# Kernel tuning notes

Hardware: AMD Instinct MI355X
Metric: run time of the kernel (lower is better)

The kernel has to match this reference:

```python
import jax, jax.numpy as jnp
import numpy as np

B, T, D = 16, 32, 4096
H, HD = 32, 128          # n_heads, head_dim
MAX_SEQ = 2048
START_POS = 1024


def _rope(x):
    # x: [b, t, h, hd]; faithful to source: positions start at 0 (no start_pos offset)
    t, hd = x.shape[1], x.shape[-1]
    theta = 10000.0 ** (-2.0 * jnp.arange(0, hd, 2, dtype=jnp.float32) / hd)  # [hd/2]
    freqs = jnp.arange(t, dtype=jnp.float32)[:, None] * theta                 # [t, hd/2]
    cos = jnp.repeat(jnp.cos(freqs), 2, axis=-1)[None, :, None, :]            # [1,t,1,hd]
    sin = jnp.repeat(jnp.sin(freqs), 2, axis=-1)[None, :, None, :]
    # rotate: even slots <- -odd, odd slots <- even (interleaved)
    x_rot = jnp.stack([-x[..., 1::2], x[..., 0::2]], axis=-1).reshape(x.shape)
    return x * cos + x_rot * sin


def setup_inputs() -> dict:
    key = jax.random.key(0)
    ks = jax.random.split(key, 7)
    s = 0.02
    return {
        "x": jax.random.normal(ks[0], (B, T, D), dtype=jnp.float32),
        "wq": jax.random.normal(ks[1], (D, D), dtype=jnp.float32) * s,
        "wk": jax.random.normal(ks[2], (D, D), dtype=jnp.float32) * s,
        "wv": jax.random.normal(ks[3], (D, D), dtype=jnp.float32) * s,
        "wo": jax.random.normal(ks[4], (D, D), dtype=jnp.float32) * s,
        "k_cache": jax.random.normal(ks[5], (B, MAX_SEQ, H, HD), dtype=jnp.float32),
        "v_cache": jax.random.normal(ks[6], (B, MAX_SEQ, H, HD), dtype=jnp.float32),
        "start_pos": START_POS,
    }


def reference(x, wq, wk, wv, wo, k_cache, v_cache, start_pos):
    b, t, _ = x.shape
    xq = (x @ wq).reshape(b, t, H, HD)
    xk = (x @ wk).reshape(b, t, H, HD)
    xv = (x @ wv).reshape(b, t, H, HD)
    xq = _rope(xq)
    xk = _rope(xk)
    # KV-cache append (start_pos is a static Python int)
    k_cache = jax.lax.dynamic_update_slice(k_cache, xk, (0, start_pos, 0, 0))
    v_cache = jax.lax.dynamic_update_slice(v_cache, xv, (0, start_pos, 0, 0))
    L = start_pos + t
    keys = k_cache[:, :L]    # [b, L, h, hd]
    values = v_cache[:, :L]
    # n_rep == 1 -> repeat_kv is identity
    scores = jnp.einsum("bthd,bshd->bhts", xq, keys) / np.float32(np.sqrt(HD))
    probs = jax.nn.softmax(scores.astype(jnp.float32), axis=-1).astype(xq.dtype)
    out = jnp.einsum("bhts,bshd->bthd", probs, values).reshape(b, t, H * HD)
    return out @ wo
```

## Files before the change

### kernel.cpp

```cpp
#include <hip/hip_runtime.h>
#include <hip/hip_bf16.h>

#define B_ 16
#define T_ 32
#define D_ 4096
#define H_ 32
#define HD_ 128
#define MAXS_ 2048
#define M_ (B_*T_)

typedef __hip_bfloat16 bf16;
typedef __attribute__((ext_vector_type(8))) short bf16x8;
typedef __attribute__((ext_vector_type(4))) float f32x4;

static __device__ __forceinline__ short f2b(float f) {
    bf16 h = __float2bfloat16(f);
    return *reinterpret_cast<short*>(&h);
}
static __device__ __forceinline__ float b2f(short s) {
    bf16 h;
    *reinterpret_cast<short*>(&h) = s;
    return __bfloat162float(h);
}

#define GLD16(gsrc, ldst) \
    __builtin_amdgcn_global_load_lds((const __attribute__((address_space(1))) void*)(gsrc), \
        (__attribute__((address_space(3))) void*)(ldst), 16, 0, 0)

__global__ __launch_bounds__(256) void conv_x(const float* __restrict__ x, bf16* __restrict__ xb) {
    int idx = blockIdx.x * 256 + threadIdx.x;
    const float4* xf = (const float4*)x;
    float4 a = xf[idx * 2], b = xf[idx * 2 + 1];
    bf16x8 o;
    o[0] = f2b(a.x); o[1] = f2b(a.y); o[2] = f2b(a.z); o[3] = f2b(a.w);
    o[4] = f2b(b.x); o[5] = f2b(b.y); o[6] = f2b(b.z); o[7] = f2b(b.w);
    *(bf16x8*)&xb[(size_t)idx * 8] = o;
}

__global__ __launch_bounds__(256) void transpose_w(const float* __restrict__ W, bf16* __restrict__ wt) {
    __shared__ float Ts[64][65];
    const int n0 = blockIdx.x * 64, k0 = blockIdx.y * 64;
    const int t = threadIdx.x;
    {
        int kk = t >> 4, nn = (t & 15) * 4;
        #pragma unroll
        for (int r = 0; r < 4; ++r) {
            float4 v = *(const float4*)&W[(size_t)(k0 + kk + 16 * r) * D_ + n0 + nn];
            Ts[kk + 16 * r][nn + 0] = v.x;
            Ts[kk + 16 * r][nn + 1] = v.y;
            Ts[kk + 16 * r][nn + 2] = v.z;
            Ts[kk + 16 * r][nn + 3] = v.w;
        }
    }
    __syncthreads();
    const int kg = t & 7, nr = t >> 3;
    #pragma unroll
    for (int r = 0; r < 2; ++r) {
        int n = nr + 32 * r;
        bf16x8 o;
        #pragma unroll
        for (int j = 0; j < 8; ++j) o[j] = f2b(Ts[kg * 8 + j][n]);
        *(bf16x8*)&wt[(size_t)(n0 + n) * D_ + k0 + kg * 8] = o;
    }
}

__global__ __launch_bounds__(256) void gemm_qkvw(const bf16* __restrict__ A,
        const float* __restrict__ wq, const float* __restrict__ wk,
        const float* __restrict__ wv, bf16* __restrict__ out) {
    const int K = D_;
    const int wsel = blockIdx.x >> 5;
    const float* W = (wsel == 0) ? wq : (wsel == 1) ? wk : wv;
    const int lcol0 = (blockIdx.x & 31) * 128;
    bf16* Ob = out + (size_t)wsel * M_ * D_;
    __shared__ bf16 As[64 * 32];
    __shared__ short Bs[128][40];
    const int tid = threadIdx.x, lane = tid & 63, wave = tid >> 6;
    const int wr = wave >> 1, wc = wave & 1;
    const int lg = lane >> 4, li = lane & 15;
    const int row0 = blockIdx.y * 64;
    const int bq = tid & 31, kq = tid >> 5;
    f32x4 acc[2][4];
    #pragma unroll
    for (int i = 0; i < 2; ++i)
        #pragma unroll
        for (int j = 0; j < 4; ++j)
            #pragma unroll
            for (int r = 0; r < 4; ++r) acc[i][j][r] = 0.f;

    const int sw = (li & 3) << 4;
    for (int k0 = 0; k0 < K; k0 += 32) {
        float4 wv4[4];
        #pragma unroll
        for (int i = 0; i < 4; ++i)
            wv4[i] = *(const float4*)&W[(size_t)(k0 + kq * 4 + i) * D_ + lcol0 + bq * 4];
        {
            int X = tid * 16;
            int row = X >> 6;
            int kb = (X & 63) ^ ((row & 3) << 4);
            GLD16(A + (size_t)(row0 + row) * K + k0 + (kb >> 1),
                  (char*)As + wave * 1024);
        }
        #pragma unroll
        for (int j = 0; j < 4; ++j) {
            int n = bq * 4 + j;
            short4 col;
            col.x = f2b(((const float*)&wv4[0])[j]);
            col.y = f2b(((const float*)&wv4[1])[j]);
            col.z = f2b(((const float*)&wv4[2])[j]);
            col.w = f2b(((const float*)&wv4[3])[j]);
            *(short4*)((char*)&Bs[n][0] + ((kq * 8) ^ (((n >> 4) & 3) << 4))) = col;
        }
        __syncthreads();
        bf16x8 af[2], bfr[4];
        #pragma unroll
        for (int i = 0; i < 2; ++i) {
            int row = wr * 32 + i * 16 + li;
            af[i] = *(const bf16x8*)((const char*)As + row * 64 + ((lg * 16) ^ sw));
        }
        #pragma unroll
        for (int j = 0; j < 4; ++j) {
            int row = wc * 64 + j * 16 + li;
            bfr[j] = *(const bf16x8*)((const char*)&Bs[row][0] + ((lg * 16) ^ (((row >> 4) & 3) << 4)));
        }
        #pragma unroll
        for (int i = 0; i < 2; ++i)
            #pragma unroll
            for (int j = 0; j < 4; ++j)
                acc[i][j] = __builtin_amdgcn_mfma_f32_16x16x32_bf16(af[i], bfr[j], acc[i][j], 0, 0, 0);
        __syncthreads();
    }
    #pragma unroll
    for (int i = 0; i < 2; ++i)
        for (int j = 0; j < 4; ++j)
            for (int r = 0; r < 4; ++r) {
                int row = row0 + wr * 32 + i * 16 + lg * 4 + r;
                int col = lcol0 + wc * 64 + j * 16 + li;
                Ob[(size_t)row * D_ + col] = __float2bfloat16(acc[i][j][r]);
            }
}

template<int BM, int BN>
__global__ __launch_bounds__(256) void gemm_bf16t(const bf16* __restrict__ A,
        const bf16* __restrict__ Bt, float* __restrict__ O) {
    constexpr int IM = BM / 32;
    constexpr int JN = BN / 32;
    constexpr int nA = (BM * 64) / 4096;
    constexpr int nB = (BN * 64) / 4096;
    const int K = D_;
    __shared__ bf16 As[BM * 32];
    __shared__ bf16 Bs[BN * 32];
    const int tid = threadIdx.x, lane = tid & 63, wave = tid >> 6;
    const int wr = wave >> 1, wc = wave & 1;
    const int lg = lane >> 4, li = lane & 15;
    const int row0 = blockIdx.y * BM, col0 = blockIdx.x * BN;
    f32x4 acc[IM][JN];
    #pragma unroll
    for (int i = 0; i < IM; ++i)
        #pragma unroll
        for (int j = 0; j < JN; ++j)
            #pragma unroll
            for (int r = 0; r < 4; ++r) acc[i][j][r] = 0.f;

    const int sw = (li & 3) << 4;
    for (int k0 = 0; k0 < K; k0 += 32) {
        #pragma unroll
        for (int i = 0; i < nA; ++i) {
            int X = (i * 256 + tid) * 16;
            int row = X >> 6;
            int kb = (X & 63) ^ ((row & 3) << 4);
            GLD16(A + (size_t)(row0 + row) * K + k0 + (kb >> 1),
                  (char*)As + (i * 256 + wave * 64) * 16);
        }
        #pragma unroll
        for (int i = 0; i < nB; ++i) {
            int X = (i * 256 + tid) * 16;
            int row = X >> 6;
            int kb = (X & 63) ^ ((row & 3) << 4);
            GLD16(Bt + (size_t)(col0 + row) * K + k0 + (kb >> 1),
                  (char*)Bs + (i * 256 + wave * 64) * 16);
        }
        __syncthreads();
        bf16x8 af[IM], bfr[JN];
        #pragma unroll
        for (int i = 0; i < IM; ++i) {
            int row = wr * (BM / 2) + i * 16 + li;
            af[i] = *(const bf16x8*)((const char*)As + row * 64 + ((lg * 16) ^ sw));
        }
        #pragma unroll
        for (int j = 0; j < JN; ++j) {
            int row = wc * (BN / 2) + j * 16 + li;
            bfr[j] = *(const bf16x8*)((const char*)Bs + row * 64 + ((lg * 16) ^ sw));
        }
        #pragma unroll
        for (int i = 0; i < IM; ++i)
            #pragma unroll
            for (int j = 0; j < JN; ++j)
                acc[i][j] = __builtin_amdgcn_mfma_f32_16x16x32_bf16(af[i], bfr[j], acc[i][j], 0, 0, 0);
        __syncthreads();
    }
    #pragma unroll
    for (int i = 0; i < IM; ++i)
        for (int j = 0; j < JN; ++j)
            for (int r = 0; r < 4; ++r) {
                int row = row0 + wr * (BM / 2) + i * 16 + lg * 4 + r;
                int col = col0 + wc * (BN / 2) + j * 16 + li;
                O[(size_t)row * D_ + col] = acc[i][j][r];
            }
}

__global__ __launch_bounds__(256) void rope_inplace(bf16* __restrict__ qb, bf16* __restrict__ kb) {
    int idx = blockIdx.x * 256 + threadIdx.x;
    size_t e0 = (size_t)idx * 8;
    int hd0 = (int)(e0 & 127);
    int t = (int)((e0 >> 12) & 31);
    bf16x8 q = *(bf16x8*)&qb[e0];
    bf16x8 k = *(bf16x8*)&kb[e0];
    bf16x8 qo, ko;
    #pragma unroll
    for (int p = 0; p < 4; ++p) {
        int i = (hd0 >> 1) + p;
        float theta = exp2f(-(float)i * 0.41524101186092787f);
        float s, c;
        sincosf((float)t * theta, &s, &c);
        float q0 = b2f(q[2 * p]), q1 = b2f(q[2 * p + 1]);
        qo[2 * p]     = f2b(q0 * c - q1 * s);
        qo[2 * p + 1] = f2b(q1 * c + q0 * s);
        float k0 = b2f(k[2 * p]), k1 = b2f(k[2 * p + 1]);
        ko[2 * p]     = f2b(k0 * c - k1 * s);
        ko[2 * p + 1] = f2b(k1 * c + k0 * s);
    }
    *(bf16x8*)&qb[e0] = qo;
    *(bf16x8*)&kb[e0] = ko;
}

__global__ __launch_bounds__(256, 3) void attn(const bf16* __restrict__ qb,
        const bf16* __restrict__ kb, const bf16* __restrict__ vb,
        const float* __restrict__ kc, const float* __restrict__ vc,
        const int* __restrict__ spp, bf16* __restrict__ ob) {
    const int bh = blockIdx.x;
    const int b = bh >> 5, h = bh & 31;
    const int sp = *spp;
    const int L = sp + T_;
    const int tid = threadIdx.x, lane = tid & 63, wave = tid >> 6;
    const int lg = lane >> 4, li = lane & 15;

    __shared__ __align__(16) char smem[52352];
    auto Vt   = (short(*)[128][40])smem;
    auto Plds = (bf16(*)[32][40])(smem + 40960);
    auto msh  = (float(*)[32])(smem + 51200);
    auto lsh  = (float(*)[32])(smem + 51712);
    float* ltot = (float*)(smem + 52224);
    float(*Osh)[128] = (float(*)[128])smem;

    bf16x8 qf[2][4];
    #pragma unroll
    for (int rt = 0; rt < 2; ++rt)
        #pragma unroll
        for (int kk = 0; kk < 4; ++kk)
            qf[rt][kk] = *(const bf16x8*)(&qb[((size_t)(b * T_ + rt * 16 + li) * H_ + h) * HD_ + kk * 32 + lg * 8]);

    f32x4 o[2][8];
    float m_r[2], l_r[2];
    m_r[0] = m_r[1] = -1e30f;
    l_r[0] = l_r[1] = 0.f;
    #pragma unroll
    for (int rt = 0; rt < 2; ++rt) for (int ht = 0; ht < 8; ++ht) for (int r = 0; r < 4; ++r) o[rt][ht][r] = 0.f;

    const float scale = 0.08838834764831845f;
    const int nch = (L + 31) >> 5;
    for (int c = wave; c < nch; c += 4) {
        const int s0 = c * 32;
        const int a = (lane >> 5) * 2;
        const int bq2 = lane & 31;
        bf16x8 kf[2][4];

        if (s0 + 32 <= sp) {
            #pragma unroll
            for (int rep = 0; rep < 2; ++rep) {
                int ao = (rep * 64 + lane) >> 5;
                int bq = (rep * 64 + lane) & 31;
                short tv[8][4];
                #pragma unroll
                for (int i = 0; i < 8; ++i) {
                    float4 v = *(const float4*)&vc[(((size_t)b * MAXS_ + s0 + ao * 8 + i) * H_ + h) * HD_ + bq * 4];
                    tv[i][0] = f2b(v.x); tv[i][1] = f2b(v.y); tv[i][2] = f2b(v.z); tv[i][3] = f2b(v.w);
                }
                #pragma unroll
                for (int j = 0; j < 4; ++j) {
                    int row = bq * 4 + j;
                    bf16x8 w;
                    #pragma unroll
                    for (int i = 0; i < 8; ++i) w[i] = tv[i][j];
                    int colB = (ao * 16) ^ (((row >> 4) & 3) << 4);
                    *(bf16x8*)((char*)&Vt[wave][row][0] + colB) = w;
                }
            }
            #pragma unroll
            for (int ct = 0; ct < 2; ++ct) {
                const float* kp = &kc[(((size_t)b * MAXS_ + s0 + ct * 16 + li) * H_ + h) * HD_];
                #pragma unroll
                for (int kk = 0; kk < 4; ++kk) {
                    float4 v0 = *(const float4*)(&kp[kk * 32 + lg * 8]);
                    float4 v1 = *(const float4*)(&kp[kk * 32 + lg * 8 + 4]);
                    bf16x8 f;
                    f[0] = f2b(v0.x); f[1] = f2b(v0.y); f[2] = f2b(v0.z); f[3] = f2b(v0.w);
                    f[4] = f2b(v1.x); f[5] = f2b(v1.y); f[6] = f2b(v1.z); f[7] = f2b(v1.w);
                    kf[ct][kk] = f;
                }
            }
        } else if (s0 >= sp) {
            #pragma unroll
            for (int rep = 0; rep < 2; ++rep) {
                int ao = (rep * 64 + lane) >> 5;
                int bq = (rep * 64 + lane) & 31;
                short tv[8][4];
                #pragma unroll
                for (int i = 0; i < 8; ++i) {
                    int s = s0 + ao * 8 + i;
                    if (s < L) {
                        ushort4 u = *(const ushort4*)&vb[(((size_t)b * T_ + (s - sp)) * H_ + h) * HD_ + bq * 4];
                        tv[i][0] = (short)u.x; tv[i][1] = (short)u.y; tv[i][2] = (short)u.z; tv[i][3] = (short)u.w;
                    } else {
                        tv[i][0] = 0; tv[i][1] = 0; tv[i][2] = 0; tv[i][3] = 0;
                    }
                }
                #pragma unroll
                for (int j = 0; j < 4; ++j) {
                    int row = bq * 4 + j;
                    bf16x8 w;
                    #pragma unroll
                    for (int i = 0; i < 8; ++i) w[i] = tv[i][j];
                    int colB = (ao * 16) ^ (((row >> 4) & 3) << 4);
                    *(bf16x8*)((char*)&Vt[wave][row][0] + colB) = w;
                }
            }
            #pragma unroll
            for (int ct = 0; ct < 2; ++ct) {
                int s = s0 + ct * 16 + li;
                if (s < L) {
                    const bf16* kp = &kb[((size_t)(b * T_ + s - sp) * H_ + h) * HD_];
                    #pragma unroll
                    for (int kk = 0; kk < 4; ++kk)
                        kf[ct][kk] = *(const bf16x8*)(kp + kk * 32 + lg * 8);
                } else {
                    #pragma unroll
                    for (int kk = 0; kk < 4; ++kk) {
                        bf16x8 f;
                        #pragma unroll
                        for (int j = 0; j < 8; ++j) f[j] = 0;
                        kf[ct][kk] = f;
                    }
                }
            }
        } else {
            #pragma unroll
            for (int rep = 0; rep < 2; ++rep) {
                int ao = (rep * 64 + lane) >> 5;
                int bq = (rep * 64 + lane) & 31;
                short tv[8][4];
                #pragma unroll
                for (int i = 0; i < 8; ++i) {
                    int s = s0 + ao * 8 + i;
                    if (s < sp) {
                        float4 v = *(const float4*)&vc[(((size_t)b * MAXS_ + s) * H_ + h) * HD_ + bq * 4];
                        tv[i][0] = f2b(v.x); tv[i][1] = f2b(v.y); tv[i][2] = f2b(v.z); tv[i][3] = f2b(v.w);
                    } else if (s < L) {
                        ushort4 u = *(const ushort4*)&vb[(((size_t)b * T_ + (s - sp)) * H_ + h) * HD_ + bq * 4];
                        tv[i][0] = (short)u.x; tv[i][1] = (short)u.y; tv[i][2] = (short)u.z; tv[i][3] = (short)u.w;
                    } else {
                        tv[i][0] = 0; tv[i][1] = 0; tv[i][2] = 0; tv[i][3] = 0;
                    }
                }
                #pragma unroll
                for (int j = 0; j < 4; ++j) {
                    int row = bq * 4 + j;
                    bf16x8 w;
                    #pragma unroll
                    for (int i = 0; i < 8; ++i) w[i] = tv[i][j];
                    int colB = (ao * 16) ^ (((row >> 4) & 3) << 4);
                    *(bf16x8*)((char*)&Vt[wave][row][0] + colB) = w;
                }
            }
            #pragma unroll
            for (int ct = 0; ct < 2; ++ct) {
                int s = s0 + ct * 16 + li;
                if (s < sp) {
                    const float* kp = &kc[(((size_t)b * MAXS_ + s) * H_ + h) * HD_];
                    #pragma unroll
                    for (int kk = 0; kk < 4; ++kk) {
                        float4 v0 = *(const float4*)(&kp[kk * 32 + lg * 8]);
                        float4 v1 = *(const float4*)(&kp[kk * 32 + lg * 8 + 4]);
                        bf16x8 f;
                        f[0] = f2b(v0.x); f[1] = f2b(v0.y); f[2] = f2b(v0.z); f[3] = f2b(v0.w);
                        f[4] = f2b(v1.x); f[5] = f2b(v1.y); f[6] = f2b(v1.z); f[7] = f2b(v1.w);
                        kf[ct][kk] = f;
                    }
                } else if (s < L) {
                    const bf16* kp = &kb[((size_t)(b * T_ + s - sp) * H_ + h) * HD_];
                    #pragma unroll
                    for (int kk = 0; kk < 4; ++kk)
                        kf[ct][kk] = *(const bf16x8*)(kp + kk * 32 + lg * 8);
                } else {
                    #pragma unroll
                    for (int kk = 0; kk < 4; ++kk) {
                        bf16x8 f;
                        #pragma unroll
                        for (int j = 0; j < 8; ++j) f[j] = 0;
                        kf[ct][kk] = f;
                    }
                }
            }
        }
        (void)a; (void)bq2;

        f32x4 sc[2][2];
        #pragma unroll
        for (int ct = 0; ct < 2; ++ct)
            #pragma unroll
            for (int rt = 0; rt < 2; ++rt) {
                f32x4 acc;
                for (int r = 0; r < 4; ++r) acc[r] = 0.f;
                #pragma unroll
                for (int kk = 0; kk < 4; ++kk)
                    acc = __builtin_amdgcn_mfma_f32_16x16x32_bf16(kf[ct][kk], qf[rt][kk], acc, 0, 0, 0);
                sc[ct][rt] = acc;
            }

        float corr[2];
        #pragma unroll
        for (int rt = 0; rt < 2; ++rt) {
            float xv[8];
            #pragma unroll
            for (int ct = 0; ct < 2; ++ct)
                #pragma unroll
                for (int r = 0; r < 4; ++r) {
                    float xx = sc[ct][rt][r] * scale;
                    if (s0 + ct * 16 + 4 * lg + r >= L) xx = -1e30f;
                    xv[ct * 4 + r] = xx;
                }
            float mx = fmaxf(fmaxf(fmaxf(xv[0], xv[1]), fmaxf(xv[2], xv[3])),
                             fmaxf(fmaxf(xv[4], xv[5]), fmaxf(xv[6], xv[7])));
            mx = fmaxf(mx, __shfl_xor(mx, 16, 64));
            mx = fmaxf(mx, __shfl_xor(mx, 32, 64));
            float mnew = fmaxf(m_r[rt], mx);
            corr[rt] = __expf(m_r[rt] - mnew);
            float p[8], ssum = 0.f;
            #pragma unroll
            for (int j = 0; j < 8; ++j) { p[j] = __expf(xv[j] - mnew); ssum += p[j]; }
            ssum += __shfl_xor(ssum, 16, 64);
            ssum += __shfl_xor(ssum, 32, 64);
            l_r[rt] = l_r[rt] * corr[rt] + ssum;
            m_r[rt] = mnew;
            #pragma unroll
            for (int ct = 0; ct < 2; ++ct)
                #pragma unroll
                for (int r = 0; r < 4; ++r)
                    Plds[wave][rt * 16 + li][ct * 16 + 4 * lg + r] = __float2bfloat16(p[ct * 4 + r]);
        }

        #pragma unroll
        for (int rt = 0; rt < 2; ++rt) {
            float cq[4];
            #pragma unroll
            for (int r = 0; r < 4; ++r) cq[r] = __shfl(corr[rt], 20 * lg + r, 64);
            #pragma unroll
            for (int ht = 0; ht < 8; ++ht)
                #pragma unroll
                for (int r = 0; r < 4; ++r) o[rt][ht][r] *= cq[r];
        }

        asm volatile("s_waitcnt lgkmcnt(0)" ::: "memory");
        bf16x8 pf[2];
        pf[0] = *(const bf16x8*)(&Plds[wave][li][lg * 8]);
        pf[1] = *(const bf16x8*)(&Plds[wave][16 + li][lg * 8]);

        #pragma unroll
        for (int ht = 0; ht < 8; ++ht) {
            int row = ht * 16 + li;
            int colB = (lg * 16) ^ ((ht & 3) << 4);
            bf16x8 vf = *(const bf16x8*)((const char*)&Vt[wave][row][0] + colB);
            #pragma unroll
            for (int rt = 0; rt < 2; ++rt)
                o[rt][ht] = __builtin_amdgcn_mfma_f32_16x16x32_bf16(pf[rt], vf, o[rt][ht], 0, 0, 0);
        }
    }

    if (lg == 0) {
        #pragma unroll
        for (int rt = 0; rt < 2; ++rt) {
            msh[wave][rt * 16 + li] = m_r[rt];
            lsh[wave][rt * 16 + li] = l_r[rt];
        }
    }
    __syncthreads();
    float corr2[2][4];
    #pragma unroll
    for (int rt = 0; rt < 2; ++rt)
        for (int r = 0; r < 4; ++r) {
            int row = rt * 16 + lg * 4 + r;
            float M = fmaxf(fmaxf(msh[0][row], msh[1][row]), fmaxf(msh[2][row], msh[3][row]));
            corr2[rt][r] = __expf(msh[wave][row] - M);
        }
    if (tid < 32) {
        int row = tid;
        float M = fmaxf(fmaxf(msh[0][row], msh[1][row]), fmaxf(msh[2][row], msh[3][row]));
        float lt = 0.f;
        #pragma unroll
        for (int w = 0; w < 4; ++w) lt += lsh[w][row] * __expf(msh[w][row] - M);
        ltot[row] = lt;
    }
    __syncthreads();
    for (int w = 0; w < 4; ++w) {
        if (wave == w) {
            #pragma unroll
            for (int rt = 0; rt < 2; ++rt)
                for (int ht = 0; ht < 8; ++ht)
                    for (int r = 0; r < 4; ++r) {
                        int row = rt * 16 + lg * 4 + r, col = ht * 16 + li;
                        float val = o[rt][ht][r] * corr2[rt][r];
                        if (w == 0) Osh[row][col] = val;
                        else Osh[row][col] += val;
                    }
        }
        __syncthreads();
    }
    {
        int row = tid >> 3;
        int c0 = (tid & 7) * 16;
        float inv = 1.0f / ltot[row];
        #pragma unroll
        for (int j = 0; j < 16; ++j)
            ob[(size_t)(b * T_ + row) * D_ + h * HD_ + c0 + j] = __float2bfloat16(Osh[row][c0 + j] * inv);
    }
}

extern "C" void kernel_launch(void* const* d_in, const int* in_sizes, int n_in,
                              void* d_out, int out_size, void* d_ws, size_t ws_size,
                              hipStream_t stream) {
    const float* x  = (const float*)d_in[0];
    const float* wq = (const float*)d_in[1];
    const float* wk = (const float*)d_in[2];
    const float* wv = (const float*)d_in[3];
    const float* wo = (const float*)d_in[4];
    const float* kc = (const float*)d_in[5];
    const float* vc = (const float*)d_in[6];
    const int*   sp = (const int*)d_in[7];

    char* ws = (char*)d_ws;
    const size_t MT = (size_t)M_ * D_;
    bf16* wt = (bf16*)ws;
    bf16* xb = wt + (size_t)D_ * D_;
    bf16* qb = xb + MT;
    bf16* kb = qb + MT;
    bf16* vb = kb + MT;
    bf16* ab = vb + MT;

    conv_x<<<dim3((int)(MT / 8 / 256)), 256, 0, stream>>>(x, xb);
    transpose_w<<<dim3(64, 64), 256, 0, stream>>>(wo, wt);
    gemm_qkvw<<<dim3(96, 8), 256, 0, stream>>>(xb, wq, wk, wv, qb);
    rope_inplace<<<dim3((int)(MT / 8 / 256)), 256, 0, stream>>>(qb, kb);
    attn<<<dim3(B_ * H_), 256, 0, stream>>>(qb, kb, vb, kc, vc, sp, ab);
    gemm_bf16t<64, 64><<<dim3(64, 8), 256, 0, stream>>>(ab, wt, (float*)d_out);
}
```

Measured before the change: 359.7 us.

## Split attention across sequence chunks with a separate combine kernel

The attention kernel now runs two blocks per (batch, head), each covering half of the KV chunks. Each block writes unnormalized fp32 partial outputs plus row max and sum. A new combine kernel rescales and merges the partials, then writes the bf16 attention output. This raises the block count to fill more compute units for the KV-cache streaming, at the cost of extra partial-buffer traffic and one more launch.

```diff
diff --git a/kernel.cpp b/kernel.cpp
--- a/kernel.cpp
+++ b/kernel.cpp
@@ -8,6 +8,7 @@
 #define HD_ 128
 #define MAXS_ 2048
 #define M_ (B_*T_)
+#define SSPLIT 2
 
 typedef __hip_bfloat16 bf16;
 typedef __attribute__((ext_vector_type(8))) short bf16x8;
@@ -236,20 +237,23 @@
 __global__ __launch_bounds__(256, 3) void attn(const bf16* __restrict__ qb,
         const bf16* __restrict__ kb, const bf16* __restrict__ vb,
         const float* __restrict__ kc, const float* __restrict__ vc,
-        const int* __restrict__ spp, bf16* __restrict__ ob) {
+        const int* __restrict__ spp,
+        float* __restrict__ pO, float* __restrict__ pml) {
     const int bh = blockIdx.x;
     const int b = bh >> 5, h = bh & 31;
+    const int split = blockIdx.y;
     const int sp = *spp;
     const int L = sp + T_;
     const int tid = threadIdx.x, lane = tid & 63, wave = tid >> 6;
     const int lg = lane >> 4, li = lane & 15;
 
-    __shared__ __align__(16) char smem[52352];
+    __shared__ __align__(16) char smem[52480];
     auto Vt   = (short(*)[128][40])smem;
     auto Plds = (bf16(*)[32][40])(smem + 40960);
     auto msh  = (float(*)[32])(smem + 51200);
     auto lsh  = (float(*)[32])(smem + 51712);
     float* ltot = (float*)(smem + 52224);
+    float* Mtot = (float*)(smem + 52352);
     float(*Osh)[128] = (float(*)[128])smem;
 
     bf16x8 qf[2][4];
@@ -268,10 +272,11 @@
 
     const float scale = 0.08838834764831845f;
     const int nch = (L + 31) >> 5;
-    for (int c = wave; c < nch; c += 4) {
+    const int per = (nch + SSPLIT - 1) / SSPLIT;
+    const int cbeg = split * per;
+    const int cend = (cbeg + per < nch) ? cbeg + per : nch;
+    for (int c = cbeg + wave; c < cend; c += 4) {
         const int s0 = c * 32;
-        const int a = (lane >> 5) * 2;
-        const int bq2 = lane & 31;
         bf16x8 kf[2][4];
 
         if (s0 + 32 <= sp) {
@@ -411,7 +416,6 @@
                 }
             }
         }
-        (void)a; (void)bq2;
 
         f32x4 sc[2][2];
         #pragma unroll
@@ -508,6 +512,7 @@
         #pragma unroll
         for (int w = 0; w < 4; ++w) lt += lsh[w][row] * __expf(msh[w][row] - M);
         ltot[row] = lt;
+        Mtot[row] = M;
     }
     __syncthreads();
     for (int w = 0; w < 4; ++w) {
@@ -525,13 +530,58 @@
         __syncthreads();
     }
     {
+        const int pbase = bh * SSPLIT + split;
         int row = tid >> 3;
         int c0 = (tid & 7) * 16;
-        float inv = 1.0f / ltot[row];
-        #pragma unroll
-        for (int j = 0; j < 16; ++j)
-            ob[(size_t)(b * T_ + row) * D_ + h * HD_ + c0 + j] = __float2bfloat16(Osh[row][c0 + j] * inv);
-    }
+        float* po = pO + ((size_t)pbase * 32 + row) * HD_ + c0;
+        #pragma unroll
+        for (int j = 0; j < 16; j += 4)
+            *(float4*)(po + j) = *(float4*)(&Osh[row][c0 + j]);
+        if (tid < 32) {
+            pml[(size_t)pbase * 64 + tid]      = Mtot[tid];
+            pml[(size_t)pbase * 64 + 32 + tid] = ltot[tid];
+        }
+    }
+}
+
+__global__ __launch_bounds__(256) void attn_combine(const float* __restrict__ pO,
+        const float* __restrict__ pml, bf16* __restrict__ ob) {
+    const int bh = blockIdx.x;
+    const int b = bh >> 5, h = bh & 31;
+    const int tid = threadIdx.x;
+    const int row = tid >> 3, c0 = (tid & 7) * 16;
+    float M = -1e30f;
+    float pm[SSPLIT], pl[SSPLIT];
+    #pragma unroll
+    for (int w = 0; w < SSPLIT; ++w) {
+        pm[w] = pml[(size_t)(bh * SSPLIT + w) * 64 + row];
+        pl[w] = pml[(size_t)(bh * SSPLIT + w) * 64 + 32 + row];
+        M = fmaxf(M, pm[w]);
+    }
+    float lt = 0.f;
+    #pragma unroll
+    for (int w = 0; w < SSPLIT; ++w) lt += pl[w] * __expf(pm[w] - M);
+    float acc[16];
+    #pragma unroll
+    for (int j = 0; j < 16; ++j) acc[j] = 0.f;
+    #pragma unroll
+    for (int w = 0; w < SSPLIT; ++w) {
+        float e = __expf(pm[w] - M);
+        const float* po = pO + ((size_t)(bh * SSPLIT + w) * 32 + row) * HD_ + c0;
+        #pragma unroll
+        for (int j = 0; j < 16; j += 4) {
+            float4 v = *(const float4*)(po + j);
+            acc[j + 0] += e * v.x; acc[j + 1] += e * v.y;
+            acc[j + 2] += e * v.z; acc[j + 3] += e * v.w;
+        }
+    }
+    float inv = 1.0f / lt;
+    bf16x8 o0, o1;
+    #pragma unroll
+    for (int j = 0; j < 8; ++j) { o0[j] = f2b(acc[j] * inv); o1[j] = f2b(acc[8 + j] * inv); }
+    bf16* dst = &ob[(size_t)(b * T_ + row) * D_ + h * HD_ + c0];
+    *(bf16x8*)dst = o0;
+    *(bf16x8*)(dst + 8) = o1;
 }
 
 extern "C" void kernel_launch(void* const* d_in, const int* in_sizes, int n_in,
@@ -554,11 +604,14 @@
     bf16* kb = qb + MT;
     bf16* vb = kb + MT;
     bf16* ab = vb + MT;
+    float* pO  = (float*)(ab + MT);
+    float* pml = pO + (size_t)B_ * H_ * SSPLIT * 32 * HD_;
 
     conv_x<<<dim3((int)(MT / 8 / 256)), 256, 0, stream>>>(x, xb);
     transpose_w<<<dim3(64, 64), 256, 0, stream>>>(wo, wt);
     gemm_qkvw<<<dim3(96, 8), 256, 0, stream>>>(xb, wq, wk, wv, qb);
     rope_inplace<<<dim3((int)(MT / 8 / 256)), 256, 0, stream>>>(qb, kb);
-    attn<<<dim3(B_ * H_), 256, 0, stream>>>(qb, kb, vb, kc, vc, sp, ab);
+    attn<<<dim3(B_ * H_, SSPLIT), 256, 0, stream>>>(qb, kb, vb, kc, vc, sp, pO, pml);
+    attn_combine<<<dim3(B_ * H_), 256, 0, stream>>>(pO, pml, ab);
     gemm_bf16t<64, 64><<<dim3(64, 8), 256, 0, stream>>>(ab, wt, (float*)d_out);
 }
```

Result: slower. 384.8 us (+7.0%).

## Software-pipeline V cache loads across chunks in attention kernel

Applied to the files above, without the earlier changes.

Splits the attention chunk loop into a pure-cache phase and a tail phase. In the cache phase, the V tile for the next chunk is prefetched into registers while the current chunk's K is converted and computed, which aims to hide global load latency. The shared compute body moves into a lambda. Launch bounds drop from 3 to 2 blocks per SM to leave room for the extra prefetch registers, at the cost of lower occupancy.

```diff
diff --git a/kernel.cpp b/kernel.cpp
--- a/kernel.cpp
+++ b/kernel.cpp
@@ -233,7 +233,7 @@
     *(bf16x8*)&kb[e0] = ko;
 }
 
-__global__ __launch_bounds__(256, 3) void attn(const bf16* __restrict__ qb,
+__global__ __launch_bounds__(256, 2) void attn(const bf16* __restrict__ qb,
         const bf16* __restrict__ kb, const bf16* __restrict__ vb,
         const float* __restrict__ kc, const float* __restrict__ vc,
         const int* __restrict__ spp, bf16* __restrict__ ob) {
@@ -243,6 +243,7 @@
     const int L = sp + T_;
     const int tid = threadIdx.x, lane = tid & 63, wave = tid >> 6;
     const int lg = lane >> 4, li = lane & 15;
+    const int a0 = lane >> 5, bq = lane & 31;
 
     __shared__ __align__(16) char smem[52352];
     auto Vt   = (short(*)[128][40])smem;
@@ -268,51 +269,146 @@
 
     const float scale = 0.08838834764831845f;
     const int nch = (L + 31) >> 5;
-    for (int c = wave; c < nch; c += 4) {
-        const int s0 = c * 32;
-        const int a = (lane >> 5) * 2;
-        const int bq2 = lane & 31;
-        bf16x8 kf[2][4];
-
-        if (s0 + 32 <= sp) {
+    const int ccache = sp >> 5;
+
+    bf16x8 kf[2][4];
+
+    auto COMPUTE = [&](int s0) {
+        f32x4 sc[2][2];
+        #pragma unroll
+        for (int ct = 0; ct < 2; ++ct)
+            #pragma unroll
+            for (int rt = 0; rt < 2; ++rt) {
+                f32x4 acc;
+                for (int r = 0; r < 4; ++r) acc[r] = 0.f;
+                #pragma unroll
+                for (int kk = 0; kk < 4; ++kk)
+                    acc = __builtin_amdgcn_mfma_f32_16x16x32_bf16(kf[ct][kk], qf[rt][kk], acc, 0, 0, 0);
+                sc[ct][rt] = acc;
+            }
+        float corr[2];
+        #pragma unroll
+        for (int rt = 0; rt < 2; ++rt) {
+            float xv[8];
+            #pragma unroll
+            for (int ct = 0; ct < 2; ++ct)
+                #pragma unroll
+                for (int r = 0; r < 4; ++r) {
+                    float xx = sc[ct][rt][r] * scale;
+                    if (s0 + ct * 16 + 4 * lg + r >= L) xx = -1e30f;
+                    xv[ct * 4 + r] = xx;
+                }
+            float mx = fmaxf(fmaxf(fmaxf(xv[0], xv[1]), fmaxf(xv[2], xv[3])),
+                             fmaxf(fmaxf(xv[4], xv[5]), fmaxf(xv[6], xv[7])));
+            mx = fmaxf(mx, __shfl_xor(mx, 16, 64));
+            mx = fmaxf(mx, __shfl_xor(mx, 32, 64));
+            float mnew = fmaxf(m_r[rt], mx);
+            corr[rt] = __expf(m_r[rt] - mnew);
+            float p[8], ssum = 0.f;
+            #pragma unroll
+            for (int j = 0; j < 8; ++j) { p[j] = __expf(xv[j] - mnew); ssum += p[j]; }
+            ssum += __shfl_xor(ssum, 16, 64);
+            ssum += __shfl_xor(ssum, 32, 64);
+            l_r[rt] = l_r[rt] * corr[rt] + ssum;
+            m_r[rt] = mnew;
+            #pragma unroll
+            for (int ct = 0; ct < 2; ++ct)
+                #pragma unroll
+                for (int r = 0; r < 4; ++r)
+                    Plds[wave][rt * 16 + li][ct * 16 + 4 * lg + r] = __float2bfloat16(p[ct * 4 + r]);
+        }
+        #pragma unroll
+        for (int rt = 0; rt < 2; ++rt) {
+            float cq[4];
+            #pragma unroll
+            for (int r = 0; r < 4; ++r) cq[r] = __shfl(corr[rt], 20 * lg + r, 64);
+            #pragma unroll
+            for (int ht = 0; ht < 8; ++ht)
+                #pragma unroll
+                for (int r = 0; r < 4; ++r) o[rt][ht][r] *= cq[r];
+        }
+        asm volatile("s_waitcnt lgkmcnt(0)" ::: "memory");
+        bf16x8 pf[2];
+        pf[0] = *(const bf16x8*)(&Plds[wave][li][lg * 8]);
+        pf[1] = *(const bf16x8*)(&Plds[wave][16 + li][lg * 8]);
+        #pragma unroll
+        for (int ht = 0; ht < 8; ++ht) {
+            int row = ht * 16 + li;
+            int colB = (lg * 16) ^ ((ht & 3) << 4);
+            bf16x8 vf = *(const bf16x8*)((const char*)&Vt[wave][row][0] + colB);
+            #pragma unroll
+            for (int rt = 0; rt < 2; ++rt)
+                o[rt][ht] = __builtin_amdgcn_mfma_f32_16x16x32_bf16(pf[rt], vf, o[rt][ht], 0, 0, 0);
+        }
+    };
+
+    int c = wave;
+    if (c < ccache) {
+        float4 vr0[8], vr1[8];
+        {
+            const float* vpB = &vc[(((size_t)b * MAXS_ + c * 32) * H_ + h) * HD_ + bq * 4];
+            #pragma unroll
+            for (int i = 0; i < 8; ++i) vr0[i] = *(const float4*)(vpB + (size_t)(a0 * 8 + i) * (H_ * HD_));
+            #pragma unroll
+            for (int i = 0; i < 8; ++i) vr1[i] = *(const float4*)(vpB + (size_t)((a0 + 2) * 8 + i) * (H_ * HD_));
+        }
+        for (;;) {
+            const int s0 = c * 32;
+            const int nc = c + 4;
+            const bool more = nc < ccache;
+            float4 kr[2][8];
+            #pragma unroll
+            for (int ct = 0; ct < 2; ++ct) {
+                const float* kp = &kc[(((size_t)b * MAXS_ + s0 + ct * 16 + li) * H_ + h) * HD_ + lg * 8];
+                #pragma unroll
+                for (int kk = 0; kk < 4; ++kk) {
+                    kr[ct][2 * kk]     = *(const float4*)(kp + kk * 32);
+                    kr[ct][2 * kk + 1] = *(const float4*)(kp + kk * 32 + 4);
+                }
+            }
             #pragma unroll
             for (int rep = 0; rep < 2; ++rep) {
-                int ao = (rep * 64 + lane) >> 5;
-                int bq = (rep * 64 + lane) & 31;
-                short tv[8][4];
-                #pragma unroll
-                for (int i = 0; i < 8; ++i) {
-                    float4 v = *(const float4*)&vc[(((size_t)b * MAXS_ + s0 + ao * 8 + i) * H_ + h) * HD_ + bq * 4];
-                    tv[i][0] = f2b(v.x); tv[i][1] = f2b(v.y); tv[i][2] = f2b(v.z); tv[i][3] = f2b(v.w);
-                }
+                const int ao = a0 + rep * 2;
                 #pragma unroll
                 for (int j = 0; j < 4; ++j) {
                     int row = bq * 4 + j;
                     bf16x8 w;
                     #pragma unroll
-                    for (int i = 0; i < 8; ++i) w[i] = tv[i][j];
+                    for (int i = 0; i < 8; ++i)
+                        w[i] = f2b(((const float*)&(rep ? vr1 : vr0)[i])[j]);
                     int colB = (ao * 16) ^ (((row >> 4) & 3) << 4);
                     *(bf16x8*)((char*)&Vt[wave][row][0] + colB) = w;
                 }
             }
-            #pragma unroll
-            for (int ct = 0; ct < 2; ++ct) {
-                const float* kp = &kc[(((size_t)b * MAXS_ + s0 + ct * 16 + li) * H_ + h) * HD_];
+            if (more) {
+                const float* vpB = &vc[(((size_t)b * MAXS_ + nc * 32) * H_ + h) * HD_ + bq * 4];
+                #pragma unroll
+                for (int i = 0; i < 8; ++i) vr0[i] = *(const float4*)(vpB + (size_t)(a0 * 8 + i) * (H_ * HD_));
+                #pragma unroll
+                for (int i = 0; i < 8; ++i) vr1[i] = *(const float4*)(vpB + (size_t)((a0 + 2) * 8 + i) * (H_ * HD_));
+            }
+            #pragma unroll
+            for (int ct = 0; ct < 2; ++ct)
                 #pragma unroll
                 for (int kk = 0; kk < 4; ++kk) {
-                    float4 v0 = *(const float4*)(&kp[kk * 32 + lg * 8]);
-                    float4 v1 = *(const float4*)(&kp[kk * 32 + lg * 8 + 4]);
                     bf16x8 f;
-                    f[0] = f2b(v0.x); f[1] = f2b(v0.y); f[2] = f2b(v0.z); f[3] = f2b(v0.w);
-                    f[4] = f2b(v1.x); f[5] = f2b(v1.y); f[6] = f2b(v1.z); f[7] = f2b(v1.w);
+                    f[0] = f2b(kr[ct][2 * kk].x); f[1] = f2b(kr[ct][2 * kk].y);
+                    f[2] = f2b(kr[ct][2 * kk].z); f[3] = f2b(kr[ct][2 * kk].w);
+                    f[4] = f2b(kr[ct][2 * kk + 1].x); f[5] = f2b(kr[ct][2 * kk + 1].y);
+                    f[6] = f2b(kr[ct][2 * kk + 1].z); f[7] = f2b(kr[ct][2 * kk + 1].w);
                     kf[ct][kk] = f;
                 }
-            }
-        } else if (s0 >= sp) {
+            COMPUTE(s0);
+            c = nc;
+            if (!more) break;
+        }
+    }
+    for (; c < nch; c += 4) {
+        const int s0 = c * 32;
+        if (s0 >= sp) {
             #pragma unroll
             for (int rep = 0; rep < 2; ++rep) {
-                int ao = (rep * 64 + lane) >> 5;
-                int bq = (rep * 64 + lane) & 31;
+                int ao = a0 + rep * 2;
                 short tv[8][4];
                 #pragma unroll
                 for (int i = 0; i < 8; ++i) {
@@ -355,8 +451,7 @@
         } else {
             #pragma unroll
             for (int rep = 0; rep < 2; ++rep) {
-                int ao = (rep * 64 + lane) >> 5;
-                int bq = (rep * 64 + lane) & 31;
+                int ao = a0 + rep * 2;
                 short tv[8][4];
                 #pragma unroll
                 for (int i = 0; i < 8; ++i) {
@@ -411,78 +506,7 @@
                 }
             }
         }
-        (void)a; (void)bq2;
-
-        f32x4 sc[2][2];
-        #pragma unroll
-        for (int ct = 0; ct < 2; ++ct)
-            #pragma unroll
-            for (int rt = 0; rt < 2; ++rt) {
-                f32x4 acc;
-                for (int r = 0; r < 4; ++r) acc[r] = 0.f;
-                #pragma unroll
-                for (int kk = 0; kk < 4; ++kk)
-                    acc = __builtin_amdgcn_mfma_f32_16x16x32_bf16(kf[ct][kk], qf[rt][kk], acc, 0, 0, 0);
-                sc[ct][rt] = acc;
-            }
-
-        float corr[2];
-        #pragma unroll
-        for (int rt = 0; rt < 2; ++rt) {
-            float xv[8];
-            #pragma unroll
-            for (int ct = 0; ct < 2; ++ct)
-                #pragma unroll
-                for (int r = 0; r < 4; ++r) {
-                    float xx = sc[ct][rt][r] * scale;
-                    if (s0 + ct * 16 + 4 * lg + r >= L) xx = -1e30f;
-                    xv[ct * 4 + r] = xx;
-                }
-            float mx = fmaxf(fmaxf(fmaxf(xv[0], xv[1]), fmaxf(xv[2], xv[3])),
-                             fmaxf(fmaxf(xv[4], xv[5]), fmaxf(xv[6], xv[7])));
-            mx = fmaxf(mx, __shfl_xor(mx, 16, 64));
-            mx = fmaxf(mx, __shfl_xor(mx, 32, 64));
-            float mnew = fmaxf(m_r[rt], mx);
-            corr[rt] = __expf(m_r[rt] - mnew);
-            float p[8], ssum = 0.f;
-            #pragma unroll
-            for (int j = 0; j < 8; ++j) { p[j] = __expf(xv[j] - mnew); ssum += p[j]; }
-            ssum += __shfl_xor(ssum, 16, 64);
-            ssum += __shfl_xor(ssum, 32, 64);
-            l_r[rt] = l_r[rt] * corr[rt] + ssum;
-            m_r[rt] = mnew;
-            #pragma unroll
-            for (int ct = 0; ct < 2; ++ct)
-                #pragma unroll
-                for (int r = 0; r < 4; ++r)
-                    Plds[wave][rt * 16 + li][ct * 16 + 4 * lg + r] = __float2bfloat16(p[ct * 4 + r]);
-        }
-
-        #pragma unroll
-        for (int rt = 0; rt < 2; ++rt) {
-            float cq[4];
-            #pragma unroll
-            for (int r = 0; r < 4; ++r) cq[r] = __shfl(corr[rt], 20 * lg + r, 64);
-            #pragma unroll
-            for (int ht = 0; ht < 8; ++ht)
-                #pragma unroll
-                for (int r = 0; r < 4; ++r) o[rt][ht][r] *= cq[r];
-        }
-
-        asm volatile("s_waitcnt lgkmcnt(0)" ::: "memory");
-        bf16x8 pf[2];
-        pf[0] = *(const bf16x8*)(&Plds[wave][li][lg * 8]);
-        pf[1] = *(const bf16x8*)(&Plds[wave][16 + li][lg * 8]);
-
-        #pragma unroll
-        for (int ht = 0; ht < 8; ++ht) {
-            int row = ht * 16 + li;
-            int colB = (lg * 16) ^ ((ht & 3) << 4);
-            bf16x8 vf = *(const bf16x8*)((const char*)&Vt[wave][row][0] + colB);
-            #pragma unroll
-            for (int rt = 0; rt < 2; ++rt)
-                o[rt][ht] = __builtin_amdgcn_mfma_f32_16x16x32_bf16(pf[rt], vf, o[rt][ht], 0, 0, 0);
-        }
+        COMPUTE(s0);
     }
 
     if (lg == 0) {
```

Result: faster. 349.2 us (-2.9%).
